# Kernel tuning notes

Measured on AMD Instinct MI355X. Metric: run time of the kernel, lower is better.

## Reference

```python
import jax, jax.numpy as jnp
import numpy as np

N_USERS = 100_000
N_ITEMS = 50_000
N_NODES = N_USERS + N_ITEMS
D = 64
K = 32          # n_intents
N_LAYERS = 2
E_UI = 1_000_000
E_UU = 500_000
E_II = 500_000


def spmm(row, col, val, x, n_rows):
    # sparse[n_rows, :] @ x via gather + segment_sum  (torch_sparse.spmm)
    return jax.ops.segment_sum(val[:, None] * x[col], row, num_segments=n_rows)


def row_normalize(row, val, n_rows):
    # D^-1 * values, matching normalization_indices_values / embed21 row scaling
    s = jax.ops.segment_sum(val, row, num_segments=n_rows)
    inv = jnp.where(s != 0, 1.0 / s, 0.0)
    return inv[row] * val


def l2norm(x):
    # F.normalize(x) along dim=1
    return x / jnp.maximum(jnp.linalg.norm(x, axis=1, keepdims=True), 1e-12)


def setup_inputs():
    key = jax.random.key(0)
    ks = jax.random.split(key, 16)
    return dict(
        user_emb=0.1 * jax.random.normal(ks[0], (N_USERS, D), jnp.float32),
        item_emb=0.1 * jax.random.normal(ks[1], (N_ITEMS, D), jnp.float32),
        intents=0.1 * jax.random.normal(ks[2], (D, K), jnp.float32),
        W2=0.1 * jax.random.normal(ks[3], (4 * D, D), jnp.float32),
        b2=jnp.zeros((D,), jnp.float32),
        uu_w=jax.random.uniform(ks[4], (E_UU,), jnp.float32),
        ii_w=jax.random.uniform(ks[5], (E_II,), jnp.float32),
        ui_u=jax.random.randint(ks[6], (E_UI,), 0, N_USERS),
        ui_i=jax.random.randint(ks[7], (E_UI,), 0, N_ITEMS),
        uu_h=jax.random.randint(ks[8], (E_UU,), 0, N_USERS),
        uu_t=jax.random.randint(ks[9], (E_UU,), 0, N_USERS),
        ii_h=jax.random.randint(ks[10], (E_II,), 0, N_ITEMS),
        ii_t=jax.random.randint(ks[11], (E_II,), 0, N_ITEMS),
    )


def reference(user_emb, item_emb, intents, W2, b2, uu_w, ii_w,
              ui_u, ui_i, uu_h, uu_t, ii_h, ii_t):
    # symmetric bipartite adjacency: (u -> n_users+i) and (n_users+i -> u)
    all_h = jnp.concatenate([ui_u, ui_i + N_USERS])
    all_t = jnp.concatenate([ui_i + N_USERS, ui_u])

    # _cal_sparse_adj: G = D^-1/2 A D^-1/2 on edge values
    deg = jax.ops.segment_sum(jnp.ones((2 * E_UI,), jnp.float32), all_h,
                              num_segments=N_NODES)
    d_inv = jnp.where(deg > 0, deg ** -0.5, 0.0)
    G_val = d_inv[all_h] * d_inv[all_t]

    # normalization_indices_values for UU / II weighted graphs (D^-1 * w)
    uu_val = row_normalize(uu_h, uu_w, N_USERS)
    ii_val = row_normalize(ii_h, ii_w, N_ITEMS)

    def embed11(x):
        return spmm(all_h, all_t, G_val, x, N_NODES)

    def embed12(x):
        u, i = x[:N_USERS], x[N_USERS:]
        return jnp.concatenate([spmm(uu_h, uu_t, uu_val, u, N_USERS),
                                spmm(ii_h, ii_t, ii_val, i, N_ITEMS)], axis=0)

    def intent_edge_weights(h_emb, t_emb, head_idx, n_heads):
        # per-edge intent distribution + alpha-weighted node aggregation
        dist = jax.nn.softmax((h_emb * t_emb) @ intents, axis=1)   # [E, K]
        alpha = (jnp.sum(h_emb * t_emb, axis=1) + 1.0) / 2.0        # [E]
        agg = jax.ops.segment_sum(alpha[:, None] * dist, head_idx,
                                  num_segments=n_heads)             # [n, K]
        recip = jnp.where(agg != 0, 1.0 / agg, 0.0)
        edge_int = alpha[:, None] * recip[head_idx]                 # [E, K]
        return jnp.mean(dist * edge_int, axis=1)                    # [E]

    def embed21(feature, x):
        h = feature[ui_u]               # [E_UI, D]
        t = feature[ui_i + N_USERS]     # [E_UI, D]
        w_u = intent_edge_weights(h, t, ui_u, N_USERS)
        w_i = intent_edge_weights(h, t, ui_i, N_ITEMS)
        w = row_normalize(all_h, jnp.concatenate([w_u, w_i]), N_NODES)
        return l2norm(spmm(all_h, all_t, w, x, N_NODES))

    def embed22(feature, x):
        uf, itf = feature[:N_USERS], feature[N_USERS:]
        ux, ix = x[:N_USERS], x[N_USERS:]
        w_uu = intent_edge_weights(uf[uu_h], uf[uu_t], uu_h, N_USERS)
        w_uu = row_normalize(uu_h, w_uu, N_USERS)
        w_ii = intent_edge_weights(itf[ii_h], itf[ii_t], ii_h, N_ITEMS)
        w_ii = row_normalize(ii_h, w_ii, N_ITEMS)
        return l2norm(jnp.concatenate([spmm(uu_h, uu_t, w_uu, ux, N_USERS),
                                       spmm(ii_h, ii_t, w_ii, ix, N_ITEMS)], axis=0))

    x = jnp.concatenate([user_emb, item_emb], axis=0)
    acc = x
    for _ in range(N_LAYERS):
        g1 = embed11(x)
        g2 = embed12(x)
        t1 = embed21(x, x)
        t2 = embed22(x, x)
        # mlp2 fusion (eval mode, dropout off): sigmoid gate over 4-way concat
        gate = jax.nn.sigmoid(jnp.concatenate([g1, g2, t1, t2], axis=1) @ W2 + b2)
        x = gate * (g1 + g2) + (1.0 - gate) * (t1 + t2)
        acc = acc + x
    return acc
```

## Files before the change

### kernel.cpp

```cpp
#include <hip/hip_runtime.h>
#include <hip/hip_fp16.h>

#define NU 100000
#define NI 50000
#define NN 150000
#define DD 64
#define KK 32
#define EUI 1000000
#define EUU 500000
#define EII 500000
#define ROWS_PB 64

static inline int cdiv(long a, int b) { return (int)((a + b - 1) / b); }

__device__ __forceinline__ float rdlane(float v, int l) {
    return __int_as_float(__builtin_amdgcn_readlane(__float_as_int(v), l));
}


__global__ void k_count(const int* __restrict__ h, int* __restrict__ cnt, int E) {
    int e = blockIdx.x * blockDim.x + threadIdx.x;
    if (e < E) atomicAdd(&cnt[h[e]], 1);
}

__global__ __launch_bounds__(1024) void k_scan(const int* __restrict__ cnt,
                                               int* __restrict__ rp, int n) {
    __shared__ int wsum[16];
    __shared__ int carry_s;
    int tid = threadIdx.x;
    int lane = tid & 63, wid = tid >> 6;
    if (tid == 0) carry_s = 0;
    __syncthreads();
    for (int base = 0; base < n; base += 1024) {
        int i = base + tid;
        int v = (i < n) ? cnt[i] : 0;
        int s = v;
#pragma unroll
        for (int off = 1; off < 64; off <<= 1) {
            int t = __shfl_up(s, off, 64);
            if (lane >= off) s += t;
        }
        if (lane == 63) wsum[wid] = s;
        __syncthreads();
        int woff = 0, total = 0;
#pragma unroll
        for (int w = 0; w < 16; w++) { int ws = wsum[w]; total += ws; if (w < wid) woff += ws; }
        int carry = carry_s;
        if (i < n) rp[i] = carry + woff + (s - v);
        __syncthreads();
        if (tid == 0) carry_s = carry + total;
        __syncthreads();
    }
    if (tid == 0) rp[n] = carry_s;
}

__global__ void k_scatter(const int* __restrict__ h, const int* __restrict__ rp,
                          int* __restrict__ cur, int* __restrict__ lst, int E) {
    int e = blockIdx.x * blockDim.x + threadIdx.x;
    if (e >= E) return;
    int r = h[e];
    int p = rp[r] + atomicAdd(&cur[r], 1);
    lst[p] = e;
}

__global__ void k_dinv(const int* __restrict__ rpu, const int* __restrict__ rpi,
                       float* __restrict__ dinv) {
    int t = blockIdx.x * blockDim.x + threadIdx.x;
    if (t >= NN) return;
    int deg = (t < NU) ? rpu[t + 1] - rpu[t] : rpi[t - NU + 1] - rpi[t - NU];
    dinv[t] = deg > 0 ? rsqrtf((float)deg) : 0.0f;
}

__global__ void k_rowsum_inv(const int* __restrict__ rp, const int* __restrict__ lst,
                             const float* __restrict__ w, float* __restrict__ out, int n) {
    int r = blockIdx.x * blockDim.x + threadIdx.x;
    if (r >= n) return;
    float s = 0.f;
    int e1 = rp[r + 1];
    for (int e = rp[r]; e < e1; e++) s += w[lst[e]];
    out[r] = (s != 0.0f) ? 1.0f / s : 0.0f;
}

__global__ void k_wdiff(const float* __restrict__ W2, float* __restrict__ Wd_g,
                        float* __restrict__ Wd_t) {
    int i = blockIdx.x * blockDim.x + threadIdx.x;
    if (i >= DD * DD) return;
    Wd_g[i] = W2[i] - W2[DD * DD + i];
    Wd_t[i] = W2[2 * DD * DD + i] - W2[3 * DD * DD + i];
}

__global__ void k_init(const float* __restrict__ ue, const float* __restrict__ ie,
                       __half* __restrict__ xh, float* __restrict__ acc) {
    size_t i = (size_t)blockIdx.x * blockDim.x + threadIdx.x;
    if (i >= (size_t)NN * DD) return;
    float v = (i < (size_t)NU * DD) ? ue[i] : ie[i - (size_t)NU * DD];
    xh[i] = __float2half(v);
    acc[i] = v;
}


__global__ void k_posU(const int* __restrict__ lst, int* __restrict__ pos, int E) {
    int p = blockIdx.x * blockDim.x + threadIdx.x;
    if (p < E) pos[lst[p]] = p;
}

__global__ void k_mapUI(const int* __restrict__ lst_i, const int* __restrict__ posU,
                        int* __restrict__ mUI, int E) {
    int p = blockIdx.x * blockDim.x + threadIdx.x;
    if (p < E) mUI[p] = posU[lst_i[p]];
}

__global__ void k_build_ui(const int* __restrict__ lst_u, const int* __restrict__ ui_u,
                           const int* __restrict__ ui_i, int* __restrict__ headU,
                           int* __restrict__ colUI, int E) {
    int p = blockIdx.x * blockDim.x + threadIdx.x;
    if (p >= E) return;
    int e = lst_u[p];
    headU[p] = ui_u[e];
    colUI[p] = ui_i[e] + NU;
}

__global__ void k_build_colI(const int* __restrict__ lst_i, const int* __restrict__ ui_u,
                             int* __restrict__ colUI, int E) {
    int p = blockIdx.x * blockDim.x + threadIdx.x;
    if (p < E) colUI[EUI + p] = ui_u[lst_i[p]];
}

__global__ void k_build_rp2(const int* __restrict__ rp_u, const int* __restrict__ rp_i,
                            const int* __restrict__ rp_uu, const int* __restrict__ rp_ii,
                            int* __restrict__ rp_ui, int* __restrict__ rp_s) {
    int t = blockIdx.x * blockDim.x + threadIdx.x;
    if (t > NN) return;
    rp_ui[t] = (t <= NU) ? rp_u[t] : rp_i[t - NU] + EUI;
    rp_s[t]  = (t <= NU) ? rp_uu[t] : rp_ii[t - NU] + EUU;
}

__global__ void k_build_gw(const int* __restrict__ rp, const int* __restrict__ col,
                           const float* __restrict__ dinv, float* __restrict__ gw, int n) {
    int r = blockIdx.x * blockDim.x + threadIdx.x;
    if (r >= n) return;
    float dh = dinv[r];
    int e1 = rp[r + 1];
    for (int p = rp[r]; p < e1; p++) gw[p] = dh * dinv[col[p]];
}

__global__ void k_build_s(const int* __restrict__ lst, const int* __restrict__ eh,
                          const int* __restrict__ et, const float* __restrict__ ew,
                          const float* __restrict__ inv, int off, int peo,
                          int* __restrict__ head, int* __restrict__ col,
                          float* __restrict__ bw, int E) {
    int p = blockIdx.x * blockDim.x + threadIdx.x;
    if (p >= E) return;
    int e = lst[p];
    int h = eh[e];
    head[peo + p] = h + off;
    col[peo + p] = et[e] + off;
    bw[peo + p] = ew[e] * inv[h];
}


__global__ __launch_bounds__(256) void k_passA(
        const int* __restrict__ head, const int* __restrict__ col,
        const __half* __restrict__ x, const float* __restrict__ intents,
        __half* __restrict__ c_out, int E) {
    __shared__ float Wl[DD * KK];
    for (int idx = threadIdx.x; idx < DD * KK; idx += blockDim.x) Wl[idx] = intents[idx];
    __syncthreads();
    int stride = gridDim.x * blockDim.x;
    for (int p = blockIdx.x * blockDim.x + threadIdx.x; p < E; p += stride) {
        const uint4* hp = (const uint4*)(x + (size_t)head[p] * DD);
        const uint4* tp = (const uint4*)(x + (size_t)col[p] * DD);
        uint4 hraw[8], traw[8];
#pragma unroll
        for (int j = 0; j < 8; j++) hraw[j] = hp[j];
#pragma unroll
        for (int j = 0; j < 8; j++) traw[j] = tp[j];
        const __half2* h2 = (const __half2*)hraw;
        const __half2* t2 = (const __half2*)traw;
        float logit[KK];
#pragma unroll
        for (int k = 0; k < KK; k++) logit[k] = 0.f;
        float dot = 0.f;
#pragma unroll 4
        for (int l4 = 0; l4 < 16; l4++) {
            float2 ha = __half22float2(h2[2 * l4]), hb = __half22float2(h2[2 * l4 + 1]);
            float2 ta = __half22float2(t2[2 * l4]), tb = __half22float2(t2[2 * l4 + 1]);
            float p0 = ha.x * ta.x, p1 = ha.y * ta.y, p2 = hb.x * tb.x, p3 = hb.y * tb.y;
            dot += p0 + p1 + p2 + p3;
            const float* w = &Wl[l4 * 4 * KK];
#pragma unroll
            for (int k = 0; k < KK; k++)
                logit[k] += p0 * w[k] + p1 * w[KK + k] + p2 * w[2 * KK + k] + p3 * w[3 * KK + k];
        }
        float m = logit[0];
#pragma unroll
        for (int k = 1; k < KK; k++) m = fmaxf(m, logit[k]);
        float ssum = 0.f;
#pragma unroll
        for (int k = 0; k < KK; k++) { float ev = __expf(logit[k] - m); logit[k] = ev; ssum += ev; }
        float scale = 0.5f * (dot + 1.0f) / ssum;
        uint4 pk[4];
        unsigned int* u = (unsigned int*)pk;
#pragma unroll
        for (int k2 = 0; k2 < 16; k2++) {
            __half2 hh = __floats2half2_rn(logit[2 * k2] * scale, logit[2 * k2 + 1] * scale);
            u[k2] = *reinterpret_cast<const unsigned int*>(&hh);
        }
        uint4* dst = (uint4*)(c_out + (size_t)p * KK);
#pragma unroll
        for (int q = 0; q < 4; q++) dst[q] = pk[q];
    }
}

__global__ __launch_bounds__(256) void k_passBC(const int* __restrict__ rp,
                                                const int* __restrict__ map,
                                                int nsplit, int peoff,
                                                const __half* __restrict__ c,
                                                float* __restrict__ w,
                                                float* __restrict__ rsinv, int n) {
    int gid = blockIdx.x * blockDim.x + threadIdx.x;
    int node = gid >> 3, j = gid & 7;
    if (node >= n) return;
    bool use_map = (map != nullptr) && (node >= nsplit);
    int p0 = rp[node], p1 = rp[node + 1];
    const uint2* cp = (const uint2*)c;
    float4 agg = make_float4(0.f, 0.f, 0.f, 0.f);
    for (int p = p0; p < p1; p++) {
        int idx = use_map ? map[p - peoff] : p;
        uint2 v = cp[(size_t)idx * 8 + j];
        float2 fa = __half22float2(*reinterpret_cast<const __half2*>(&v.x));
        float2 fb = __half22float2(*reinterpret_cast<const __half2*>(&v.y));
        agg.x += fa.x; agg.y += fa.y; agg.z += fb.x; agg.w += fb.y;
    }
    float4 rec;
    rec.x = (agg.x != 0.f) ? 1.f / agg.x : 0.f;
    rec.y = (agg.y != 0.f) ? 1.f / agg.y : 0.f;
    rec.z = (agg.z != 0.f) ? 1.f / agg.z : 0.f;
    rec.w = (agg.w != 0.f) ? 1.f / agg.w : 0.f;
    float rs = 0.f;
    for (int p = p0; p < p1; p++) {
        int idx = use_map ? map[p - peoff] : p;
        uint2 v = cp[(size_t)idx * 8 + j];
        float2 fa = __half22float2(*reinterpret_cast<const __half2*>(&v.x));
        float2 fb = __half22float2(*reinterpret_cast<const __half2*>(&v.y));
        float dot = fa.x * rec.x + fa.y * rec.y + fb.x * rec.z + fb.y * rec.w;
        dot += __shfl_xor(dot, 1, 64);
        dot += __shfl_xor(dot, 2, 64);
        dot += __shfl_xor(dot, 4, 64);
        float wv = dot * (1.0f / KK);
        if (j == 0) w[p] = wv;
        rs += wv;
    }
    if (j == 0) rsinv[node] = (rs != 0.f) ? 1.f / rs : 0.f;
}

#define PRD(a0, a1, a2, a3, l) \
    rdlane(((l) & 3) == 0 ? (a0) : ((l) & 3) == 1 ? (a1) : ((l) & 3) == 2 ? (a2) : (a3), (l) >> 2)

__global__ __launch_bounds__(512) void k_fused_ui(
        const int* __restrict__ rp, const int* __restrict__ col,
        const float* __restrict__ gw, const float* __restrict__ w,
        const float* __restrict__ rsinv, const float* __restrict__ Wd_g,
        const float* __restrict__ Wd_t, const float* __restrict__ b2,
        const __half* __restrict__ x, float* __restrict__ gs, float* __restrict__ ts,
        float* __restrict__ zp, int nrows) {
    __shared__ float Wg[DD * DD];
    __shared__ float Wt[DD * DD];
    for (int i = threadIdx.x; i < DD * DD; i += 512) { Wg[i] = Wd_g[i]; Wt[i] = Wd_t[i]; }
    __syncthreads();
    int wid = threadIdx.x >> 6, lane = threadIdx.x & 63;
    int sub = lane & 15, grp = lane >> 4;
    float b2v = b2[lane];
    const uint2* xq = (const uint2*)x;
    int rbase = blockIdx.x * ROWS_PB + wid * 8;
    for (int rr = 0; rr < 8; rr++) {
        int r = rbase + rr;
        if (r >= nrows) break;
        float g0 = 0, g1 = 0, g2 = 0, g3 = 0, t0 = 0, t1 = 0, t2 = 0, t3 = 0;
        int e = rp[r], e1 = rp[r + 1];
        for (; e + 8 <= e1; e += 8) {
#pragma unroll
            for (int u = 0; u < 2; u++) {
                int idx = e + 4 * u + grp;
                int cc = col[idx];
                float wg = gw[idx], wt = w[idx];
                uint2 raw = xq[(size_t)cc * 16 + sub];
                float2 xa = __half22float2(*(const __half2*)&raw.x);
                float2 xb = __half22float2(*(const __half2*)&raw.y);
                g0 += wg * xa.x; g1 += wg * xa.y; g2 += wg * xb.x; g3 += wg * xb.y;
                t0 += wt * xa.x; t1 += wt * xa.y; t2 += wt * xb.x; t3 += wt * xb.y;
            }
        }
        for (; e < e1; e += 4) {
            int idx = e + grp;
            if (idx < e1) {
                int cc = col[idx];
                float wg = gw[idx], wt = w[idx];
                uint2 raw = xq[(size_t)cc * 16 + sub];
                float2 xa = __half22float2(*(const __half2*)&raw.x);
                float2 xb = __half22float2(*(const __half2*)&raw.y);
                g0 += wg * xa.x; g1 += wg * xa.y; g2 += wg * xb.x; g3 += wg * xb.y;
                t0 += wt * xa.x; t1 += wt * xa.y; t2 += wt * xb.x; t3 += wt * xb.y;
            }
        }
#pragma unroll
        for (int off = 16; off <= 32; off <<= 1) {
            g0 += __shfl_xor(g0, off, 64); g1 += __shfl_xor(g1, off, 64);
            g2 += __shfl_xor(g2, off, 64); g3 += __shfl_xor(g3, off, 64);
            t0 += __shfl_xor(t0, off, 64); t1 += __shfl_xor(t1, off, 64);
            t2 += __shfl_xor(t2, off, 64); t3 += __shfl_xor(t3, off, 64);
        }
        float rsv = rsinv[r];
        t0 *= rsv; t1 *= rsv; t2 *= rsv; t3 *= rsv;
        float ss = t0 * t0 + t1 * t1 + t2 * t2 + t3 * t3;
        ss += __shfl_xor(ss, 1, 64); ss += __shfl_xor(ss, 2, 64);
        ss += __shfl_xor(ss, 4, 64); ss += __shfl_xor(ss, 8, 64);
        float inv_n = 1.0f / fmaxf(sqrtf(ss), 1e-12f);
        t0 *= inv_n; t1 *= inv_n; t2 *= inv_n; t3 *= inv_n;
        float zv = b2v;
#pragma unroll
        for (int l = 0; l < DD; l++) {
            float gl = PRD(g0, g1, g2, g3, l);
            float tl = PRD(t0, t1, t2, t3, l);
            zv += gl * Wg[l * DD + lane] + tl * Wt[l * DD + lane];
        }
        float ga0 = __shfl(g0, lane >> 2, 64), ga1 = __shfl(g1, lane >> 2, 64);
        float ga2 = __shfl(g2, lane >> 2, 64), ga3 = __shfl(g3, lane >> 2, 64);
        float ta0 = __shfl(t0, lane >> 2, 64), ta1 = __shfl(t1, lane >> 2, 64);
        float ta2 = __shfl(t2, lane >> 2, 64), ta3 = __shfl(t3, lane >> 2, 64);
        int j = lane & 3;
        float gsv = j == 0 ? ga0 : j == 1 ? ga1 : j == 2 ? ga2 : ga3;
        float tsv = j == 0 ? ta0 : j == 1 ? ta1 : j == 2 ? ta2 : ta3;
        size_t oi = (size_t)r * DD + lane;
        gs[oi] = gsv;
        ts[oi] = tsv;
        zp[oi] = zv;
    }
}

__global__ __launch_bounds__(512) void k_fused_fin(
        const int* __restrict__ rp, const int* __restrict__ col,
        const float* __restrict__ bw, const float* __restrict__ w,
        const float* __restrict__ rsinv,
        const float* __restrict__ W1, const float* __restrict__ W3,
        const __half* __restrict__ x, const float* __restrict__ gs,
        const float* __restrict__ ts, const float* __restrict__ zp,
        __half* __restrict__ xh_out, float* __restrict__ acc, int nrows) {
    __shared__ float Wa[DD * DD];
    __shared__ float Wb[DD * DD];
    for (int i = threadIdx.x; i < DD * DD; i += 512) { Wa[i] = W1[i]; Wb[i] = W3[i]; }
    __syncthreads();
    int wid = threadIdx.x >> 6, lane = threadIdx.x & 63;
    int sub = lane & 15, grp = lane >> 4;
    const uint2* xq = (const uint2*)x;
    int rbase = blockIdx.x * ROWS_PB + wid * 8;
    for (int rr = 0; rr < 8; rr++) {
        int r = rbase + rr;
        if (r >= nrows) break;
        float g0 = 0, g1 = 0, g2 = 0, g3 = 0, t0 = 0, t1 = 0, t2 = 0, t3 = 0;
        int e = rp[r], e1 = rp[r + 1];
        for (; e + 8 <= e1; e += 8) {
#pragma unroll
            for (int u = 0; u < 2; u++) {
                int idx = e + 4 * u + grp;
                int cc = col[idx];
                float wg = bw[idx], wt = w[idx];
                uint2 raw = xq[(size_t)cc * 16 + sub];
                float2 xa = __half22float2(*(const __half2*)&raw.x);
                float2 xb = __half22float2(*(const __half2*)&raw.y);
                g0 += wg * xa.x; g1 += wg * xa.y; g2 += wg * xb.x; g3 += wg * xb.y;
                t0 += wt * xa.x; t1 += wt * xa.y; t2 += wt * xb.x; t3 += wt * xb.y;
            }
        }
        for (; e < e1; e += 4) {
            int idx = e + grp;
            if (idx < e1) {
                int cc = col[idx];
                float wg = bw[idx], wt = w[idx];
                uint2 raw = xq[(size_t)cc * 16 + sub];
                float2 xa = __half22float2(*(const __half2*)&raw.x);
                float2 xb = __half22float2(*(const __half2*)&raw.y);
                g0 += wg * xa.x; g1 += wg * xa.y; g2 += wg * xb.x; g3 += wg * xb.y;
                t0 += wt * xa.x; t1 += wt * xa.y; t2 += wt * xb.x; t3 += wt * xb.y;
            }
        }
#pragma unroll
        for (int off = 16; off <= 32; off <<= 1) {
            g0 += __shfl_xor(g0, off, 64); g1 += __shfl_xor(g1, off, 64);
            g2 += __shfl_xor(g2, off, 64); g3 += __shfl_xor(g3, off, 64);
            t0 += __shfl_xor(t0, off, 64); t1 += __shfl_xor(t1, off, 64);
            t2 += __shfl_xor(t2, off, 64); t3 += __shfl_xor(t3, off, 64);
        }
        float rsv = rsinv[r];
        t0 *= rsv; t1 *= rsv; t2 *= rsv; t3 *= rsv;
        float ss = t0 * t0 + t1 * t1 + t2 * t2 + t3 * t3;
        ss += __shfl_xor(ss, 1, 64); ss += __shfl_xor(ss, 2, 64);
        ss += __shfl_xor(ss, 4, 64); ss += __shfl_xor(ss, 8, 64);
        float inv_n = 1.0f / fmaxf(sqrtf(ss), 1e-12f);
        t0 *= inv_n; t1 *= inv_n; t2 *= inv_n; t3 *= inv_n;
        float4 gp = ((const float4*)(gs + (size_t)r * DD))[sub];
        float4 tp = ((const float4*)(ts + (size_t)r * DD))[sub];
        float gf0 = gp.x + g0, gf1 = gp.y + g1, gf2 = gp.z + g2, gf3 = gp.w + g3;
        float tf0 = tp.x + t0, tf1 = tp.y + t1, tf2 = tp.z + t2, tf3 = tp.w + t3;
        size_t oi = (size_t)r * DD + lane;
        float zv = zp[oi];
#pragma unroll
        for (int l = 0; l < DD; l++) {
            float gl = PRD(gf0, gf1, gf2, gf3, l);
            float tl = PRD(tf0, tf1, tf2, tf3, l);
            zv += gl * Wa[l * DD + lane] + tl * Wb[l * DD + lane];
        }
        float ga0 = __shfl(gf0, lane >> 2, 64), ga1 = __shfl(gf1, lane >> 2, 64);
        float ga2 = __shfl(gf2, lane >> 2, 64), ga3 = __shfl(gf3, lane >> 2, 64);
        float ta0 = __shfl(tf0, lane >> 2, 64), ta1 = __shfl(tf1, lane >> 2, 64);
        float ta2 = __shfl(tf2, lane >> 2, 64), ta3 = __shfl(tf3, lane >> 2, 64);
        int j = lane & 3;
        float gfin = j == 0 ? ga0 : j == 1 ? ga1 : j == 2 ? ga2 : ga3;
        float tfin = j == 0 ? ta0 : j == 1 ? ta1 : j == 2 ? ta2 : ta3;
        float gate = 1.0f / (1.0f + __expf(-zv));
        float xn = gate * gfin + (1.0f - gate) * tfin;
        xh_out[oi] = __float2half(xn);
        acc[oi] += xn;
    }
}


extern "C" void kernel_launch(void* const* d_in, const int* in_sizes, int n_in,
                              void* d_out, int out_size, void* d_ws, size_t ws_size,
                              hipStream_t stream) {
    const float* user_emb = (const float*)d_in[0];
    const float* item_emb = (const float*)d_in[1];
    const float* intents  = (const float*)d_in[2];
    const float* W2       = (const float*)d_in[3];
    const float* b2       = (const float*)d_in[4];
    const float* uu_w     = (const float*)d_in[5];
    const float* ii_w     = (const float*)d_in[6];
    const int*   ui_u     = (const int*)d_in[7];
    const int*   ui_i     = (const int*)d_in[8];
    const int*   uu_h     = (const int*)d_in[9];
    const int*   uu_t     = (const int*)d_in[10];
    const int*   ii_h     = (const int*)d_in[11];
    const int*   ii_t     = (const int*)d_in[12];
    float* acc = (float*)d_out;

    char* pw = (char*)d_ws;
    auto allocb = [&](size_t nbytes) -> char* {
        char* r = pw;
        pw += (nbytes + 255) & ~(size_t)255;
        return r;
    };
    float* gs    = (float*)allocb((size_t)NN * DD * 4);
    float* ts    = (float*)allocb((size_t)NN * DD * 4);
    float* zp    = (float*)allocb((size_t)NN * DD * 4);
    __half* xh0  = (__half*)allocb((size_t)NN * DD * 2);
    __half* xh1  = (__half*)allocb((size_t)NN * DD * 2);
    __half* c    = (__half*)allocb((size_t)EUI * KK * 2);
    float* w     = (float*)allocb((size_t)2 * EUI * 4);
    float* rs    = (float*)allocb((size_t)NN * 4);
    float* dinv  = (float*)allocb((size_t)NN * 4);
    float* iuu   = (float*)allocb((size_t)NU * 4);
    float* iii   = (float*)allocb((size_t)NI * 4);
    float* Wd_g  = (float*)allocb((size_t)DD * DD * 4);
    float* Wd_t  = (float*)allocb((size_t)DD * DD * 4);
    int* rp_u    = (int*)allocb(((size_t)NU + 1) * 4);
    int* rp_i    = (int*)allocb(((size_t)NI + 1) * 4);
    int* rp_uu   = (int*)allocb(((size_t)NU + 1) * 4);
    int* rp_ii   = (int*)allocb(((size_t)NI + 1) * 4);
    int* rp_ui   = (int*)allocb(((size_t)NN + 1) * 4);
    int* rp_s    = (int*)allocb(((size_t)NN + 1) * 4);
    int* headU   = (int*)allocb((size_t)EUI * 4);
    int* colUI   = (int*)allocb((size_t)2 * EUI * 4);
    int* head_s  = (int*)allocb((size_t)(EUU + EII) * 4);
    int* col_s   = (int*)allocb((size_t)(EUU + EII) * 4);
    float* bw_s  = (float*)allocb((size_t)(EUU + EII) * 4);
    int* mUI     = (int*)allocb((size_t)EUI * 4);
    float* gwUI  = (float*)allocb((size_t)2 * EUI * 4);

    char* ca = (char*)c;
    int* cur    = (int*)ca;  ca += ((size_t)NU * 4 + 255) & ~(size_t)255;
    int* lst_u  = (int*)ca;  ca += ((size_t)EUI * 4 + 255) & ~(size_t)255;
    int* lst_i  = (int*)ca;  ca += ((size_t)EUI * 4 + 255) & ~(size_t)255;
    int* lst_uu = (int*)ca;  ca += ((size_t)EUU * 4 + 255) & ~(size_t)255;
    int* lst_ii = (int*)ca;  ca += ((size_t)EII * 4 + 255) & ~(size_t)255;
    int* posU   = (int*)ca;

    const int B = 256;

    auto build_csr = [&](const int* h, int E, int n, int* rp, int* lst) {
        hipMemsetAsync(cur, 0, (size_t)n * 4, stream);
        k_count<<<cdiv(E, B), B, 0, stream>>>(h, cur, E);
        k_scan<<<1, 1024, 0, stream>>>(cur, rp, n);
        hipMemsetAsync(cur, 0, (size_t)n * 4, stream);
        k_scatter<<<cdiv(E, B), B, 0, stream>>>(h, rp, cur, lst, E);
    };

    build_csr(ui_u, EUI, NU, rp_u, lst_u);
    build_csr(ui_i, EUI, NI, rp_i, lst_i);
    build_csr(uu_h, EUU, NU, rp_uu, lst_uu);
    build_csr(ii_h, EII, NI, rp_ii, lst_ii);
    k_dinv<<<cdiv(NN, B), B, 0, stream>>>(rp_u, rp_i, dinv);
    k_rowsum_inv<<<cdiv(NU, B), B, 0, stream>>>(rp_uu, lst_uu, uu_w, iuu, NU);
    k_rowsum_inv<<<cdiv(NI, B), B, 0, stream>>>(rp_ii, lst_ii, ii_w, iii, NI);
    k_build_rp2<<<cdiv(NN + 1, B), B, 0, stream>>>(rp_u, rp_i, rp_uu, rp_ii, rp_ui, rp_s);
    k_build_ui<<<cdiv(EUI, B), B, 0, stream>>>(lst_u, ui_u, ui_i, headU, colUI, EUI);
    k_build_colI<<<cdiv(EUI, B), B, 0, stream>>>(lst_i, ui_u, colUI, EUI);
    k_posU<<<cdiv(EUI, B), B, 0, stream>>>(lst_u, posU, EUI);
    k_mapUI<<<cdiv(EUI, B), B, 0, stream>>>(lst_i, posU, mUI, EUI);
    k_build_s<<<cdiv(EUU, B), B, 0, stream>>>(lst_uu, uu_h, uu_t, uu_w, iuu, 0, 0,
                                              head_s, col_s, bw_s, EUU);
    k_build_s<<<cdiv(EII, B), B, 0, stream>>>(lst_ii, ii_h, ii_t, ii_w, iii, NU, EUU,
                                              head_s, col_s, bw_s, EII);
    k_build_gw<<<cdiv(NN, B), B, 0, stream>>>(rp_ui, colUI, dinv, gwUI, NN);
    k_wdiff<<<cdiv(DD * DD, B), B, 0, stream>>>(W2, Wd_g, Wd_t);
    k_init<<<cdiv((long)NN * DD, B), B, 0, stream>>>(user_emb, item_emb, xh0, acc);

    for (int layer = 0; layer < 2; ++layer) {
        const __half* xin = (layer == 0) ? xh0 : xh1;
        __half* xout = (layer == 0) ? xh1 : xh0;

        k_passA<<<1024, B, 0, stream>>>(headU, colUI, xin, intents, c, EUI);
        k_passBC<<<cdiv((long)NN * 8, B), B, 0, stream>>>(rp_ui, mUI, NU, EUI, c, w, rs, NN);
        k_fused_ui<<<cdiv(NN, ROWS_PB), 512, 0, stream>>>(rp_ui, colUI, gwUI, w, rs,
                                                          Wd_g, Wd_t, b2, xin, gs, ts, zp, NN);

        k_passA<<<1024, B, 0, stream>>>(head_s, col_s, xin, intents, c, EUU + EII);
        k_passBC<<<cdiv((long)NN * 8, B), B, 0, stream>>>(rp_s, nullptr, 0, 0, c, w, rs, NN);
        k_fused_fin<<<cdiv(NN, ROWS_PB), 512, 0, stream>>>(rp_s, col_s, bw_s, w, rs,
                                                           W2 + DD * DD, W2 + 3 * DD * DD,
                                                           xin, gs, ts, zp, xout, acc, NN);
    }
}
```

Measured before the change: 2.248 ms.

## Fuse intent edge-weight computation into SpMM kernels and store gs/ts in fp16

The second pass of k_passBC, which recomputed per-edge intent weights and row sums into a global w/rs buffer, is removed. k_passB now only writes per-node reciprocal intent sums (32 floats per node). The fused SpMM kernels re-read the fp16 intent vectors per edge and compute the edge weight and row sum inline. This saves one full re-read of c plus the w/rs write and read traffic, at the cost of an extra 128-byte per-node recip buffer and more shuffles inside the gather loop. The gs/ts intermediates are also halved to fp16, which cuts bandwidth but adds some precision loss.

```diff
diff --git a/kernel.cpp b/kernel.cpp
--- a/kernel.cpp
+++ b/kernel.cpp
@@ -212,12 +212,11 @@
     }
 }
 
-__global__ __launch_bounds__(256) void k_passBC(const int* __restrict__ rp,
-                                                const int* __restrict__ map,
-                                                int nsplit, int peoff,
-                                                const __half* __restrict__ c,
-                                                float* __restrict__ w,
-                                                float* __restrict__ rsinv, int n) {
+__global__ __launch_bounds__(256) void k_passB(const int* __restrict__ rp,
+                                               const int* __restrict__ map,
+                                               int nsplit, int peoff,
+                                               const __half* __restrict__ c,
+                                               float* __restrict__ recip, int n) {
     int gid = blockIdx.x * blockDim.x + threadIdx.x;
     int node = gid >> 3, j = gid & 7;
     if (node >= n) return;
@@ -237,21 +236,7 @@
     rec.y = (agg.y != 0.f) ? 1.f / agg.y : 0.f;
     rec.z = (agg.z != 0.f) ? 1.f / agg.z : 0.f;
     rec.w = (agg.w != 0.f) ? 1.f / agg.w : 0.f;
-    float rs = 0.f;
-    for (int p = p0; p < p1; p++) {
-        int idx = use_map ? map[p - peoff] : p;
-        uint2 v = cp[(size_t)idx * 8 + j];
-        float2 fa = __half22float2(*reinterpret_cast<const __half2*>(&v.x));
-        float2 fb = __half22float2(*reinterpret_cast<const __half2*>(&v.y));
-        float dot = fa.x * rec.x + fa.y * rec.y + fb.x * rec.z + fb.y * rec.w;
-        dot += __shfl_xor(dot, 1, 64);
-        dot += __shfl_xor(dot, 2, 64);
-        dot += __shfl_xor(dot, 4, 64);
-        float wv = dot * (1.0f / KK);
-        if (j == 0) w[p] = wv;
-        rs += wv;
-    }
-    if (j == 0) rsinv[node] = (rs != 0.f) ? 1.f / rs : 0.f;
+    ((float4*)recip)[(size_t)node * 8 + j] = rec;
 }
 
 #define PRD(a0, a1, a2, a3, l) \
@@ -259,10 +244,11 @@
 
 __global__ __launch_bounds__(512) void k_fused_ui(
         const int* __restrict__ rp, const int* __restrict__ col,
-        const float* __restrict__ gw, const float* __restrict__ w,
-        const float* __restrict__ rsinv, const float* __restrict__ Wd_g,
-        const float* __restrict__ Wd_t, const float* __restrict__ b2,
-        const __half* __restrict__ x, float* __restrict__ gs, float* __restrict__ ts,
+        const float* __restrict__ gw, const __half* __restrict__ cbuf,
+        const int* __restrict__ mUI, const float* __restrict__ recip,
+        const float* __restrict__ Wd_g, const float* __restrict__ Wd_t,
+        const float* __restrict__ b2, const __half* __restrict__ x,
+        __half* __restrict__ gs, __half* __restrict__ ts,
         float* __restrict__ zp, int nrows) {
     __shared__ float Wg[DD * DD];
     __shared__ float Wt[DD * DD];
@@ -272,18 +258,30 @@
     int sub = lane & 15, grp = lane >> 4;
     float b2v = b2[lane];
     const uint2* xq = (const uint2*)x;
+    const unsigned int* cu = (const unsigned int*)cbuf;
     int rbase = blockIdx.x * ROWS_PB + wid * 8;
     for (int rr = 0; rr < 8; rr++) {
         int r = rbase + rr;
         if (r >= nrows) break;
+        float2 rc = *(const float2*)(recip + (size_t)r * KK + 2 * sub);
+        bool item = (r >= NU);
         float g0 = 0, g1 = 0, g2 = 0, g3 = 0, t0 = 0, t1 = 0, t2 = 0, t3 = 0;
+        float rsacc = 0.f;
         int e = rp[r], e1 = rp[r + 1];
         for (; e + 8 <= e1; e += 8) {
 #pragma unroll
             for (int u = 0; u < 2; u++) {
                 int idx = e + 4 * u + grp;
                 int cc = col[idx];
-                float wg = gw[idx], wt = w[idx];
+                float wg = gw[idx];
+                int ci = item ? mUI[idx - EUI] : idx;
+                unsigned int cv = cu[(size_t)ci * 16 + sub];
+                float2 cf = __half22float2(*(const __half2*)&cv);
+                float pd = fmaf(cf.x, rc.x, cf.y * rc.y);
+                pd += __shfl_xor(pd, 1, 64); pd += __shfl_xor(pd, 2, 64);
+                pd += __shfl_xor(pd, 4, 64); pd += __shfl_xor(pd, 8, 64);
+                float wt = pd * (1.0f / KK);
+                rsacc += wt;
                 uint2 raw = xq[(size_t)cc * 16 + sub];
                 float2 xa = __half22float2(*(const __half2*)&raw.x);
                 float2 xb = __half22float2(*(const __half2*)&raw.y);
@@ -295,7 +293,15 @@
             int idx = e + grp;
             if (idx < e1) {
                 int cc = col[idx];
-                float wg = gw[idx], wt = w[idx];
+                float wg = gw[idx];
+                int ci = item ? mUI[idx - EUI] : idx;
+                unsigned int cv = cu[(size_t)ci * 16 + sub];
+                float2 cf = __half22float2(*(const __half2*)&cv);
+                float pd = fmaf(cf.x, rc.x, cf.y * rc.y);
+                pd += __shfl_xor(pd, 1, 64); pd += __shfl_xor(pd, 2, 64);
+                pd += __shfl_xor(pd, 4, 64); pd += __shfl_xor(pd, 8, 64);
+                float wt = pd * (1.0f / KK);
+                rsacc += wt;
                 uint2 raw = xq[(size_t)cc * 16 + sub];
                 float2 xa = __half22float2(*(const __half2*)&raw.x);
                 float2 xb = __half22float2(*(const __half2*)&raw.y);
@@ -309,8 +315,9 @@
             g2 += __shfl_xor(g2, off, 64); g3 += __shfl_xor(g3, off, 64);
             t0 += __shfl_xor(t0, off, 64); t1 += __shfl_xor(t1, off, 64);
             t2 += __shfl_xor(t2, off, 64); t3 += __shfl_xor(t3, off, 64);
-        }
-        float rsv = rsinv[r];
+            rsacc += __shfl_xor(rsacc, off, 64);
+        }
+        float rsv = (rsacc != 0.f) ? 1.0f / rsacc : 0.f;
         t0 *= rsv; t1 *= rsv; t2 *= rsv; t3 *= rsv;
         float ss = t0 * t0 + t1 * t1 + t2 * t2 + t3 * t3;
         ss += __shfl_xor(ss, 1, 64); ss += __shfl_xor(ss, 2, 64);
@@ -332,19 +339,19 @@
         float gsv = j == 0 ? ga0 : j == 1 ? ga1 : j == 2 ? ga2 : ga3;
         float tsv = j == 0 ? ta0 : j == 1 ? ta1 : j == 2 ? ta2 : ta3;
         size_t oi = (size_t)r * DD + lane;
-        gs[oi] = gsv;
-        ts[oi] = tsv;
+        gs[oi] = __float2half(gsv);
+        ts[oi] = __float2half(tsv);
         zp[oi] = zv;
     }
 }
 
 __global__ __launch_bounds__(512) void k_fused_fin(
         const int* __restrict__ rp, const int* __restrict__ col,
-        const float* __restrict__ bw, const float* __restrict__ w,
-        const float* __restrict__ rsinv,
+        const float* __restrict__ bw, const __half* __restrict__ cbuf,
+        const float* __restrict__ recip,
         const float* __restrict__ W1, const float* __restrict__ W3,
-        const __half* __restrict__ x, const float* __restrict__ gs,
-        const float* __restrict__ ts, const float* __restrict__ zp,
+        const __half* __restrict__ x, const __half* __restrict__ gs,
+        const __half* __restrict__ ts, const float* __restrict__ zp,
         __half* __restrict__ xh_out, float* __restrict__ acc, int nrows) {
     __shared__ float Wa[DD * DD];
     __shared__ float Wb[DD * DD];
@@ -353,18 +360,28 @@
     int wid = threadIdx.x >> 6, lane = threadIdx.x & 63;
     int sub = lane & 15, grp = lane >> 4;
     const uint2* xq = (const uint2*)x;
+    const unsigned int* cu = (const unsigned int*)cbuf;
     int rbase = blockIdx.x * ROWS_PB + wid * 8;
     for (int rr = 0; rr < 8; rr++) {
         int r = rbase + rr;
         if (r >= nrows) break;
+        float2 rc = *(const float2*)(recip + (size_t)r * KK + 2 * sub);
         float g0 = 0, g1 = 0, g2 = 0, g3 = 0, t0 = 0, t1 = 0, t2 = 0, t3 = 0;
+        float rsacc = 0.f;
         int e = rp[r], e1 = rp[r + 1];
         for (; e + 8 <= e1; e += 8) {
 #pragma unroll
             for (int u = 0; u < 2; u++) {
                 int idx = e + 4 * u + grp;
                 int cc = col[idx];
-                float wg = bw[idx], wt = w[idx];
+                float wg = bw[idx];
+                unsigned int cv = cu[(size_t)idx * 16 + sub];
+                float2 cf = __half22float2(*(const __half2*)&cv);
+                float pd = fmaf(cf.x, rc.x, cf.y * rc.y);
+                pd += __shfl_xor(pd, 1, 64); pd += __shfl_xor(pd, 2, 64);
+                pd += __shfl_xor(pd, 4, 64); pd += __shfl_xor(pd, 8, 64);
+                float wt = pd * (1.0f / KK);
+                rsacc += wt;
                 uint2 raw = xq[(size_t)cc * 16 + sub];
                 float2 xa = __half22float2(*(const __half2*)&raw.x);
                 float2 xb = __half22float2(*(const __half2*)&raw.y);
@@ -376,7 +393,14 @@
             int idx = e + grp;
             if (idx < e1) {
                 int cc = col[idx];
-                float wg = bw[idx], wt = w[idx];
+                float wg = bw[idx];
+                unsigned int cv = cu[(size_t)idx * 16 + sub];
+                float2 cf = __half22float2(*(const __half2*)&cv);
+                float pd = fmaf(cf.x, rc.x, cf.y * rc.y);
+                pd += __shfl_xor(pd, 1, 64); pd += __shfl_xor(pd, 2, 64);
+                pd += __shfl_xor(pd, 4, 64); pd += __shfl_xor(pd, 8, 64);
+                float wt = pd * (1.0f / KK);
+                rsacc += wt;
                 uint2 raw = xq[(size_t)cc * 16 + sub];
                 float2 xa = __half22float2(*(const __half2*)&raw.x);
                 float2 xb = __half22float2(*(const __half2*)&raw.y);
@@ -390,18 +414,23 @@
             g2 += __shfl_xor(g2, off, 64); g3 += __shfl_xor(g3, off, 64);
             t0 += __shfl_xor(t0, off, 64); t1 += __shfl_xor(t1, off, 64);
             t2 += __shfl_xor(t2, off, 64); t3 += __shfl_xor(t3, off, 64);
-        }
-        float rsv = rsinv[r];
+            rsacc += __shfl_xor(rsacc, off, 64);
+        }
+        float rsv = (rsacc != 0.f) ? 1.0f / rsacc : 0.f;
         t0 *= rsv; t1 *= rsv; t2 *= rsv; t3 *= rsv;
         float ss = t0 * t0 + t1 * t1 + t2 * t2 + t3 * t3;
         ss += __shfl_xor(ss, 1, 64); ss += __shfl_xor(ss, 2, 64);
         ss += __shfl_xor(ss, 4, 64); ss += __shfl_xor(ss, 8, 64);
         float inv_n = 1.0f / fmaxf(sqrtf(ss), 1e-12f);
         t0 *= inv_n; t1 *= inv_n; t2 *= inv_n; t3 *= inv_n;
-        float4 gp = ((const float4*)(gs + (size_t)r * DD))[sub];
-        float4 tp = ((const float4*)(ts + (size_t)r * DD))[sub];
-        float gf0 = gp.x + g0, gf1 = gp.y + g1, gf2 = gp.z + g2, gf3 = gp.w + g3;
-        float tf0 = tp.x + t0, tf1 = tp.y + t1, tf2 = tp.z + t2, tf3 = tp.w + t3;
+        uint2 gp2 = ((const uint2*)(gs + (size_t)r * DD))[sub];
+        uint2 tp2 = ((const uint2*)(ts + (size_t)r * DD))[sub];
+        float2 gpa = __half22float2(*(const __half2*)&gp2.x);
+        float2 gpb = __half22float2(*(const __half2*)&gp2.y);
+        float2 tpa = __half22float2(*(const __half2*)&tp2.x);
+        float2 tpb = __half22float2(*(const __half2*)&tp2.y);
+        float gf0 = gpa.x + g0, gf1 = gpa.y + g1, gf2 = gpb.x + g2, gf3 = gpb.y + g3;
+        float tf0 = tpa.x + t0, tf1 = tpa.y + t1, tf2 = tpb.x + t2, tf3 = tpb.y + t3;
         size_t oi = (size_t)r * DD + lane;
         float zv = zp[oi];
 #pragma unroll
@@ -449,14 +478,13 @@
         pw += (nbytes + 255) & ~(size_t)255;
         return r;
     };
-    float* gs    = (float*)allocb((size_t)NN * DD * 4);
-    float* ts    = (float*)allocb((size_t)NN * DD * 4);
+    __half* gs   = (__half*)allocb((size_t)NN * DD * 2);
+    __half* ts   = (__half*)allocb((size_t)NN * DD * 2);
     float* zp    = (float*)allocb((size_t)NN * DD * 4);
     __half* xh0  = (__half*)allocb((size_t)NN * DD * 2);
     __half* xh1  = (__half*)allocb((size_t)NN * DD * 2);
     __half* c    = (__half*)allocb((size_t)EUI * KK * 2);
-    float* w     = (float*)allocb((size_t)2 * EUI * 4);
-    float* rs    = (float*)allocb((size_t)NN * 4);
+    float* recip = (float*)allocb((size_t)NN * KK * 4);
     float* dinv  = (float*)allocb((size_t)NN * 4);
     float* iuu   = (float*)allocb((size_t)NU * 4);
     float* iii   = (float*)allocb((size_t)NI * 4);
@@ -519,13 +547,13 @@
         __half* xout = (layer == 0) ? xh1 : xh0;
 
         k_passA<<<1024, B, 0, stream>>>(headU, colUI, xin, intents, c, EUI);
-        k_passBC<<<cdiv((long)NN * 8, B), B, 0, stream>>>(rp_ui, mUI, NU, EUI, c, w, rs, NN);
-        k_fused_ui<<<cdiv(NN, ROWS_PB), 512, 0, stream>>>(rp_ui, colUI, gwUI, w, rs,
+        k_passB<<<cdiv((long)NN * 8, B), B, 0, stream>>>(rp_ui, mUI, NU, EUI, c, recip, NN);
+        k_fused_ui<<<cdiv(NN, ROWS_PB), 512, 0, stream>>>(rp_ui, colUI, gwUI, c, mUI, recip,
                                                           Wd_g, Wd_t, b2, xin, gs, ts, zp, NN);
 
         k_passA<<<1024, B, 0, stream>>>(head_s, col_s, xin, intents, c, EUU + EII);
-        k_passBC<<<cdiv((long)NN * 8, B), B, 0, stream>>>(rp_s, nullptr, 0, 0, c, w, rs, NN);
-        k_fused_fin<<<cdiv(NN, ROWS_PB), 512, 0, stream>>>(rp_s, col_s, bw_s, w, rs,
+        k_passB<<<cdiv((long)NN * 8, B), B, 0, stream>>>(rp_s, nullptr, 0, 0, c, recip, NN);
+        k_fused_fin<<<cdiv(NN, ROWS_PB), 512, 0, stream>>>(rp_s, col_s, bw_s, c, recip,
                                                            W2 + DD * DD, W2 + 3 * DD * DD,
                                                            xin, gs, ts, zp, xout, acc, NN);
     }
```

Measured after the change: 2.234 ms. No clear change (-0.6%).
